# Kernel tuning notes

Hardware: AMD Instinct MI355X
Metric: run time of the kernel (lower is better)

Reference implementation:

```python
import jax, jax.numpy as jnp
import numpy as np

NEG_SLOPE = 0.01

def setup_inputs() -> dict:
    key = jax.random.key(0)
    ks = jax.random.split(key, 6)
    B, N, IN, OUT = 4, 4096, 256, 128
    x = jax.random.normal(ks[0], (B, N, IN), dtype=jnp.float32)
    # fc: Linear(in, out, bias=False); attn_l/attn_r: Linear(out, 1) with bias
    W_fc = jax.random.normal(ks[1], (IN, OUT), dtype=jnp.float32) / np.sqrt(IN)
    w_l = jax.random.normal(ks[2], (OUT,), dtype=jnp.float32) / np.sqrt(OUT)
    b_l = jax.random.normal(ks[3], (), dtype=jnp.float32) * 0.01
    w_r = jax.random.normal(ks[4], (OUT,), dtype=jnp.float32) / np.sqrt(OUT)
    b_r = jax.random.normal(ks[5], (), dtype=jnp.float32) * 0.01
    return {"x": x, "W_fc": W_fc, "w_l": w_l, "b_l": b_l, "w_r": w_r, "b_r": b_r}

def reference(x, W_fc, w_l, b_l, w_r, b_r):
    # feats: [B, N, OUT]
    feats = jnp.einsum('bni,io->bno', x, W_fc)
    f1 = jnp.einsum('bno,o->bn', feats, w_l) + b_l  # [B, N]
    f2 = jnp.einsum('bno,o->bn', feats, w_r) + b_r  # [B, N]
    # logits[b, i, j] = f1[b, i] + f2[b, j]  (broadcast-add)
    logits = f1[:, :, None] + f2[:, None, :]        # [B, N, N]
    scores = jnp.where(logits >= 0, logits, NEG_SLOPE * logits)
    coefs = jax.nn.softmax(scores, axis=1)          # softmax over dim=1, as in torch code
    return jnp.einsum('bij,bjo->bio', coefs, feats) # [B, N, OUT]
```

## Files before the change

### kernel.cpp

```cpp
#include <hip/hip_runtime.h>

using u16 = unsigned short;
using u32 = unsigned int;
using u64 = unsigned long long;

typedef short bf16x8 __attribute__((ext_vector_type(8)));
typedef float f32x4 __attribute__((ext_vector_type(4)));

static constexpr int NB  = 4;
static constexpr int NN  = 4096;
static constexpr int KIN = 256;
static constexpr int FO  = 128;
static constexpr int NROW = NB * NN;
static constexpr int NCC = 64;
static constexpr float SLOPE = 0.01f;

__device__ __forceinline__ u16 f2bf(float f) {
  const u32 u = __float_as_uint(f);
  return (u16)((u + 0x7fffu + ((u >> 16) & 1u)) >> 16);
}
__device__ __forceinline__ float bf2f(u16 h) {
  return __uint_as_float(((u32)h) << 16);
}
__device__ __forceinline__ float dot4(const float4& a, const float4& b) {
  return a.x * b.x + a.y * b.y + a.z * b.z + a.w * b.w;
}

__device__ __forceinline__ u32 f2key(float f) {
  const u32 b = __float_as_uint(f);
  return (b & 0x80000000u) ? ~b : (b | 0x80000000u);
}
__device__ __forceinline__ float key2f(u32 u) {
  const u32 b = (u & 0x80000000u) ? (u ^ 0x80000000u) : ~u;
  return __uint_as_float(b);
}

__device__ __forceinline__ u64 shfl_xor64(u64 v, int m) {
  const u32 lo = __shfl_xor((u32)(v & 0xffffffffu), m, 64);
  const u32 hi = __shfl_xor((u32)(v >> 32), m, 64);
  return ((u64)hi << 32) | (u64)lo;
}
__device__ __forceinline__ void cswap(u64& a, u64& b, bool up) {
  if ((a > b) == up) { const u64 tmp = a; a = b; b = tmp; }
}

__device__ __forceinline__ void reg_session(u64 e[4], int t, int k) {
  const int jstart = (k > 256) ? 128 : (k >> 1);
  for (int j = jstart; j >= 4; j >>= 1) {
    const int J = j >> 2;
    const bool up   = ((t & (k >> 2)) == 0);
    const bool lowr = ((t & J) == 0);
#pragma unroll
    for (int r = 0; r < 4; ++r) {
      const u64 o = shfl_xor64(e[r], J);
      const bool less = e[r] < o;
      e[r] = ((lowr == up) == less) ? e[r] : o;
    }
  }
  if (k >= 4) {
    const bool up = ((t & (k >> 2)) == 0);
    cswap(e[0], e[2], up); cswap(e[1], e[3], up);
  }
  {
    const bool up0 = (((4 * t)     & k) == 0);
    const bool up1 = (((4 * t + 2) & k) == 0);
    cswap(e[0], e[1], up0); cswap(e[2], e[3], up1);
  }
}

__global__ __launch_bounds__(256) void k0_prep(const float* __restrict__ W,
                                               const float* __restrict__ wl,
                                               const float* __restrict__ wr,
                                               float* __restrict__ u_l,
                                               float* __restrict__ u_r,
                                               u16* __restrict__ whT,
                                               u16* __restrict__ wloT) {
  const int t = threadIdx.x;
  const int blk = blockIdx.x;
  if (blk < 64) {
    const int k = blk * 4 + (t >> 6);
    const int lane = t & 63;
    const float w0 = W[k * FO + lane], w1 = W[k * FO + 64 + lane];
    float a1 = w0 * wl[lane] + w1 * wl[64 + lane];
    float a2 = w0 * wr[lane] + w1 * wr[64 + lane];
#pragma unroll
    for (int off = 1; off < 64; off <<= 1) {
      a1 += __shfl_xor(a1, off, 64);
      a2 += __shfl_xor(a2, off, 64);
    }
    if (lane == 0) { u_l[k] = a1; u_r[k] = a2; }
  } else {
#pragma unroll
    for (int e = 0; e < 2; ++e) {
      const int idx = (blk - 64) * 512 + t + e * 256;
      const int col = idx >> 8, k = idx & 255;
      const float v = W[k * FO + col];
      const u16 h = f2bf(v);
      whT[col * KIN + k]  = h;
      wloT[col * KIN + k] = f2bf(v - bf2f(h));
    }
  }
}

__global__ __launch_bounds__(256) void k1_fused(const float* __restrict__ x,
                                                const u16* __restrict__ whT,
                                                const u16* __restrict__ wloT,
                                                const float* __restrict__ u_l,
                                                const float* __restrict__ u_r,
                                                const float* __restrict__ blp,
                                                const float* __restrict__ brp,
                                                float* __restrict__ feats,
                                                float* __restrict__ f1g,
                                                float* __restrict__ f2g) {
  __shared__ u16 axh[64][72];
  __shared__ u16 axl[64][72];
  __shared__ u16 bwh[128][72];
  __shared__ u16 bwl[128][72];
  const int t = threadIdx.x;
  const int w = t >> 6, lane = t & 63;
  const int wm = w >> 1, wn = w & 1;
  const int row0 = blockIdx.x * 64;
  const int xr = t >> 3, xc = t & 7;
  f32x4 acc[2][4];
#pragma unroll
  for (int m = 0; m < 2; ++m)
#pragma unroll
    for (int n = 0; n < 4; ++n) acc[m][n] = (f32x4)0.f;

  float d1a = 0.f, d2a = 0.f, d1b = 0.f, d2b = 0.f;
  float4 xa0, xa1, xb0, xb1;
  bf16x8 wh_[4], wl_[4];

  {
    const float* pa = x + (size_t)(row0 + xr) * KIN + xc * 8;
    const float* pb = x + (size_t)(row0 + xr + 32) * KIN + xc * 8;
    xa0 = *(const float4*)pa; xa1 = *(const float4*)(pa + 4);
    xb0 = *(const float4*)pb; xb1 = *(const float4*)(pb + 4);
#pragma unroll
    for (int i = 0; i < 4; ++i) {
      const int v = t + i * 256;
      const int col = v >> 3, c = v & 7;
      wh_[i] = *(const bf16x8*)(whT + (size_t)col * KIN + c * 8);
      wl_[i] = *(const bf16x8*)(wloT + (size_t)col * KIN + c * 8);
    }
  }

  for (int it = 0; it < 4; ++it) {
    if (it) __syncthreads();
    {
      const float4 ul0 = *(const float4*)(u_l + it * 64 + xc * 8);
      const float4 ul1 = *(const float4*)(u_l + it * 64 + xc * 8 + 4);
      const float4 ur0 = *(const float4*)(u_r + it * 64 + xc * 8);
      const float4 ur1 = *(const float4*)(u_r + it * 64 + xc * 8 + 4);
      d1a += dot4(xa0, ul0) + dot4(xa1, ul1);
      d2a += dot4(xa0, ur0) + dot4(xa1, ur1);
      d1b += dot4(xb0, ul0) + dot4(xb1, ul1);
      d2b += dot4(xb0, ur0) + dot4(xb1, ur1);
    }
    {
      float va[8] = {xa0.x, xa0.y, xa0.z, xa0.w, xa1.x, xa1.y, xa1.z, xa1.w};
      float vb[8] = {xb0.x, xb0.y, xb0.z, xb0.w, xb1.x, xb1.y, xb1.z, xb1.w};
      bf16x8 ha, la, hb, lb;
#pragma unroll
      for (int q = 0; q < 8; ++q) {
        const u16 h1 = f2bf(va[q]);
        ha[q] = (short)h1; la[q] = (short)f2bf(va[q] - bf2f(h1));
        const u16 h2 = f2bf(vb[q]);
        hb[q] = (short)h2; lb[q] = (short)f2bf(vb[q] - bf2f(h2));
      }
      *(bf16x8*)(&axh[xr][xc * 8]) = ha;
      *(bf16x8*)(&axl[xr][xc * 8]) = la;
      *(bf16x8*)(&axh[xr + 32][xc * 8]) = hb;
      *(bf16x8*)(&axl[xr + 32][xc * 8]) = lb;
    }
#pragma unroll
    for (int i = 0; i < 4; ++i) {
      const int v = t + i * 256;
      const int col = v >> 3, c = v & 7;
      *(bf16x8*)(&bwh[col][c * 8]) = wh_[i];
      *(bf16x8*)(&bwl[col][c * 8]) = wl_[i];
    }
    __syncthreads();
    if (it < 3) {
      const float* pa = x + (size_t)(row0 + xr) * KIN + (it + 1) * 64 + xc * 8;
      const float* pb = x + (size_t)(row0 + xr + 32) * KIN + (it + 1) * 64 + xc * 8;
      xa0 = *(const float4*)pa; xa1 = *(const float4*)(pa + 4);
      xb0 = *(const float4*)pb; xb1 = *(const float4*)(pb + 4);
#pragma unroll
      for (int i = 0; i < 4; ++i) {
        const int v = t + i * 256;
        const int col = v >> 3, c = v & 7;
        wh_[i] = *(const bf16x8*)(whT + (size_t)col * KIN + (it + 1) * 64 + c * 8);
        wl_[i] = *(const bf16x8*)(wloT + (size_t)col * KIN + (it + 1) * 64 + c * 8);
      }
    }
#pragma unroll
    for (int kk = 0; kk < 2; ++kk) {
      const int kb = kk * 32 + (lane >> 4) * 8;
      bf16x8 ah[2], al[2], bh[4], blo[4];
#pragma unroll
      for (int m = 0; m < 2; ++m) {
        const int r = wm * 32 + m * 16 + (lane & 15);
        ah[m] = *(const bf16x8*)(&axh[r][kb]);
        al[m] = *(const bf16x8*)(&axl[r][kb]);
      }
#pragma unroll
      for (int n = 0; n < 4; ++n) {
        const int cidx = wn * 64 + n * 16 + (lane & 15);
        bh[n]  = *(const bf16x8*)(&bwh[cidx][kb]);
        blo[n] = *(const bf16x8*)(&bwl[cidx][kb]);
      }
#pragma unroll
      for (int m = 0; m < 2; ++m)
#pragma unroll
        for (int n = 0; n < 4; ++n) {
          acc[m][n] = __builtin_amdgcn_mfma_f32_16x16x32_bf16(ah[m], bh[n],  acc[m][n], 0, 0, 0);
          acc[m][n] = __builtin_amdgcn_mfma_f32_16x16x32_bf16(ah[m], blo[n], acc[m][n], 0, 0, 0);
          acc[m][n] = __builtin_amdgcn_mfma_f32_16x16x32_bf16(al[m], bh[n],  acc[m][n], 0, 0, 0);
        }
    }
  }

#pragma unroll
  for (int m = 0; m < 2; ++m) {
    const int rb = row0 + wm * 32 + m * 16 + (lane >> 4) * 4;
    const int cb = wn * 64 + (lane & 15);
#pragma unroll
    for (int n = 0; n < 4; ++n)
#pragma unroll
      for (int r = 0; r < 4; ++r)
        feats[(size_t)(rb + r) * FO + cb + n * 16] = acc[m][n][r];
  }

#pragma unroll
  for (int off = 1; off < 8; off <<= 1) {
    d1a += __shfl_xor(d1a, off, 64);
    d2a += __shfl_xor(d2a, off, 64);
    d1b += __shfl_xor(d1b, off, 64);
    d2b += __shfl_xor(d2b, off, 64);
  }
  if ((t & 7) == 0) {
    const float bl = blp[0], br = brp[0];
    f1g[row0 + xr] = d1a + bl;
    f2g[row0 + xr] = d2a + br;
    f1g[row0 + xr + 32] = d1b + bl;
    f2g[row0 + xr + 32] = d2b + br;
  }
}

__global__ __launch_bounds__(1024, 1) void k3a_sort(const float* __restrict__ f1g,
                                                    const float* __restrict__ f2g,
                                                    float* __restrict__ f1sort,
                                                    float* __restrict__ sc1,
                                                    float* __restrict__ sc2,
                                                    float* __restrict__ f2sort,
                                                    int* __restrict__ jidxS) {
  __shared__ u64 lds[NN];
  __shared__ float wsumA[16], wsumB[16];
  const int t = threadIdx.x;
  const int lane = t & 63, wv = t >> 6;
  const int b = blockIdx.x & 3;
  const int task = blockIdx.x >> 2;
  const int base = b * NN;
  const float* __restrict__ src = task ? f2g : f1g;

  u64 e[4];
#pragma unroll
  for (int r = 0; r < 4; ++r) {
    const int i = 4 * t + r;
    e[r] = ((u64)f2key(src[base + i]) << 32) | (u32)i;
  }

  for (int k = 2; k <= 256; k <<= 1) reg_session(e, t, k);
#pragma unroll
  for (int r = 0; r < 4; ++r) lds[4 * t + r] = e[r];
  __syncthreads();

  for (int k = 512; k <= NN; k <<= 1) {
    for (int j = k >> 1; j >= 256; j >>= 1) {
#pragma unroll
      for (int pp = 0; pp < 2; ++pp) {
        const int p = t + pp * 1024;
        const int i = ((p & ~(j - 1)) << 1) | (p & (j - 1));
        const int ix = i | j;
        const bool up = ((i & k) == 0);
        const u64 a = lds[i], c = lds[ix];
        if ((a > c) == up) { lds[i] = c; lds[ix] = a; }
      }
      __syncthreads();
    }
#pragma unroll
    for (int r = 0; r < 4; ++r) e[r] = lds[4 * t + r];
    reg_session(e, t, k);
    if (k < NN) {
#pragma unroll
      for (int r = 0; r < 4; ++r) lds[4 * t + r] = e[r];
      __syncthreads();
    }
  }

  if (task == 0) {
    float kf[4], a[4], c[4];
#pragma unroll
    for (int r = 0; r < 4; ++r) {
      kf[r] = key2f((u32)(e[r] >> 32));
      f1sort[base + 4 * t + r] = kf[r];
      a[r] = expf(kf[r]);
      c[r] = expf(SLOPE * kf[r]);
    }
#pragma unroll
    for (int r = 1; r < 4; ++r) { a[r] += a[r - 1]; c[r] += c[r - 1]; }
    const float sa = a[3], sb = c[3];
    float pa = sa, pb = sb;
    for (int off = 1; off < 64; off <<= 1) {
      const float oa = __shfl_up(pa, off, 64);
      const float ob = __shfl_up(pb, off, 64);
      if (lane >= off) { pa += oa; pb += ob; }
    }
    if (lane == 63) { wsumA[wv] = pa; wsumB[wv] = pb; }
    __syncthreads();
    float wpa = 0.f, wpb = 0.f;
    for (int w2 = 0; w2 < wv; ++w2) { wpa += wsumA[w2]; wpb += wsumB[w2]; }
    const float basea = wpa + pa - sa, baseb = wpb + pb - sb;
#pragma unroll
    for (int r = 0; r < 4; ++r) {
      sc1[base + 4 * t + r] = basea + a[r];
      sc2[base + 4 * t + r] = baseb + c[r];
    }
  } else {
#pragma unroll
    for (int r = 0; r < 4; ++r) {
      f2sort[base + 4 * t + r] = key2f((u32)(e[r] >> 32));
      jidxS[base + 4 * t + r]  = (int)(e[r] & 0xffffffffu);
    }
  }
}

__device__ __forceinline__ int lower_bound_s(const float* a, int n, float t) {
  int lo = 0, hi = n;
  while (lo < hi) {
    const int mid = (lo + hi) >> 1;
    if (a[mid] < t) lo = mid + 1; else hi = mid;
  }
  return lo;
}

__global__ __launch_bounds__(512) void k3b_ab(const float* __restrict__ f1sort,
                                              const float* __restrict__ sc1,
                                              const float* __restrict__ sc2,
                                              const float* __restrict__ f2sort,
                                              const float* __restrict__ f1g,
                                              float* __restrict__ alphaS,
                                              float* __restrict__ betaS,
                                              int* __restrict__ kposA,
                                              float* __restrict__ E1g,
                                              float* __restrict__ E2g) {
  __shared__ float s_f1[NN];
  __shared__ float s_f2[NN];
  const int b = blockIdx.x >> 3;
  const int part = blockIdx.x & 7;
  const int base = b * NN;
  for (int i = threadIdx.x; i < NN; i += 512) {
    s_f1[i] = f1sort[base + i];
    s_f2[i] = f2sort[base + i];
  }
  __syncthreads();
  const int g = part * 512 + threadIdx.x;
  const float T1 = sc1[base + NN - 1];
  const float f1max = s_f1[NN - 1];
  {
    const float f2v = s_f2[g];
    const float m = f1max + f2v;
    const float M = (m >= 0.f) ? m : SLOPE * m;
    const int p = lower_bound_s(s_f1, NN, -f2v);
    const float S1 = T1 - (p > 0 ? sc1[base + p - 1] : 0.f);
    const float S2 = (p > 0 ? sc2[base + p - 1] : 0.f);
    const float ea = expf(f2v - M);
    const float eb = expf(SLOPE * f2v - M);
    const float invD = 1.0f / (ea * S1 + eb * S2);
    alphaS[base + g] = ea * invD;
    betaS[base + g]  = eb * invD;
  }
  {
    const float f1v = f1g[base + g];
    kposA[base + g] = lower_bound_s(s_f2, NN, -f1v);
    E1g[base + g] = expf(f1v);
    E2g[base + g] = expf(SLOPE * f1v);
  }
}

__global__ __launch_bounds__(128) void k4a_pref(const float* __restrict__ feats,
                                                const float* __restrict__ alphaS,
                                                const float* __restrict__ betaS,
                                                const int* __restrict__ jidxS,
                                                float* __restrict__ finePreA,
                                                float* __restrict__ finePreB) {
  const int b = blockIdx.x >> 6, cc = blockIdx.x & 63;
  const int o = threadIdx.x;
  const int base = b * NN + cc * 64;
  const float* fb = feats + (size_t)b * NN * FO;
  float accA = 0.f, accB = 0.f;
#pragma unroll 8
  for (int q = 0; q < 64; ++q) {
    const int kk = base + q;
    const int j = jidxS[kk];
    const float fv = fb[(size_t)j * FO + o];
    accA = fmaf(alphaS[kk], fv, accA);
    accB = fmaf(betaS[kk], fv, accB);
    finePreA[(size_t)kk * FO + o] = accA;
    finePreB[(size_t)kk * FO + o] = accB;
  }
}

__global__ __launch_bounds__(128) void k4c_coar(const float* __restrict__ finePreA,
                                                const float* __restrict__ finePreB,
                                                float* __restrict__ coarA,
                                                float* __restrict__ coarB) {
  const int b = blockIdx.x;
  const int o = threadIdx.x;
  float runA = 0.f, runB = 0.f;
#pragma unroll
  for (int c = 0; c < NCC; ++c) {
    coarA[(size_t)(b * (NCC + 1) + c) * FO + o] = runA;
    coarB[(size_t)(b * (NCC + 1) + c) * FO + o] = runB;
    runA += finePreA[(size_t)(b * NN + c * 64 + 63) * FO + o];
    runB += finePreB[(size_t)(b * NN + c * 64 + 63) * FO + o];
  }
  coarA[(size_t)(b * (NCC + 1) + NCC) * FO + o] = runA;
  coarB[(size_t)(b * (NCC + 1) + NCC) * FO + o] = runB;
}

__global__ __launch_bounds__(256) void k5_out(const float* __restrict__ finePreA,
                                              const float* __restrict__ finePreB,
                                              const float* __restrict__ coarA,
                                              const float* __restrict__ coarB,
                                              const int* __restrict__ kposA,
                                              const float* __restrict__ E1g,
                                              const float* __restrict__ E2g,
                                              float* __restrict__ out) {
  const int t = threadIdx.x;
  const int row = blockIdx.x * 2 + (t >> 7);
  const int o = t & 127;
  const int b = row >> 12;
  const int kp = kposA[row];
  const float e1 = E1g[row], e2 = E2g[row];
  const int c = kp >> 6;

  float runA = coarA[(size_t)(b * (NCC + 1) + c) * FO + o];
  float runB = coarB[(size_t)(b * (NCC + 1) + c) * FO + o];
  const float totA = coarA[(size_t)(b * (NCC + 1) + NCC) * FO + o];
  if (kp & 63) {
    runA += finePreA[(size_t)(b * NN + kp - 1) * FO + o];
    runB += finePreB[(size_t)(b * NN + kp - 1) * FO + o];
  }
  out[(size_t)row * FO + o] = fmaf(e1, totA - runA, e2 * runB);
}

extern "C" void kernel_launch(void* const* d_in, const int* in_sizes, int n_in,
                              void* d_out, int out_size, void* d_ws, size_t ws_size,
                              hipStream_t stream) {
  const float* x  = (const float*)d_in[0];
  const float* W  = (const float*)d_in[1];
  const float* wl = (const float*)d_in[2];
  const float* bl = (const float*)d_in[3];
  const float* wr = (const float*)d_in[4];
  const float* br = (const float*)d_in[5];
  float* out = (float*)d_out;

  float* ws = (float*)d_ws;
  float* feats    = ws; ws += NROW * FO;
  float* finePreA = ws; ws += NROW * FO;
  float* finePreB = ws; ws += NROW * FO;
  float* f1g      = ws; ws += NROW;
  float* f2g      = ws; ws += NROW;
  float* f1sort   = ws; ws += NROW;
  float* f2sort   = ws; ws += NROW;
  float* sc1      = ws; ws += NROW;
  float* sc2      = ws; ws += NROW;
  float* alphaS   = ws; ws += NROW;
  float* betaS    = ws; ws += NROW;
  float* E1g      = ws; ws += NROW;
  float* E2g      = ws; ws += NROW;
  int* jidxS      = (int*)ws; ws += NROW;
  int* kposA      = (int*)ws; ws += NROW;
  float* coarA    = ws; ws += NB * (NCC + 1) * FO;
  float* coarB    = ws; ws += NB * (NCC + 1) * FO;
  float* u_l      = ws; ws += KIN;
  float* u_r      = ws; ws += KIN;
  u16* whT  = (u16*)ws; ws += FO * KIN / 2;
  u16* wloT = (u16*)ws; ws += FO * KIN / 2;
  (void)in_sizes; (void)n_in; (void)out_size; (void)ws_size;

  hipLaunchKernelGGL(k0_prep,  dim3(128),       dim3(256),  0, stream,
                     W, wl, wr, u_l, u_r, whT, wloT);
  hipLaunchKernelGGL(k1_fused, dim3(NROW / 64), dim3(256),  0, stream,
                     x, whT, wloT, u_l, u_r, bl, br, feats, f1g, f2g);
  hipLaunchKernelGGL(k3a_sort, dim3(8),         dim3(1024), 0, stream,
                     f1g, f2g, f1sort, sc1, sc2, f2sort, jidxS);
  hipLaunchKernelGGL(k3b_ab,   dim3(NB * 8),    dim3(512),  0, stream,
                     f1sort, sc1, sc2, f2sort, f1g, alphaS, betaS, kposA, E1g, E2g);
  hipLaunchKernelGGL(k4a_pref, dim3(NB * NCC),  dim3(128),  0, stream,
                     feats, alphaS, betaS, jidxS, finePreA, finePreB);
  hipLaunchKernelGGL(k4c_coar, dim3(NB),        dim3(128),  0, stream,
                     finePreA, finePreB, coarA, coarB);
  hipLaunchKernelGGL(k5_out,   dim3(NROW / 2),  dim3(256),  0, stream,
                     finePreA, finePreB, coarA, coarB, kposA, E1g, E2g, out);
}
```

Before: 68.51 us.

## Overlap f1/f2 sort with feature GEMM by merging into one heterogeneous kernel

After: 70.77 us. 1.03x slower.

```diff
diff --git a/kernel.cpp b/kernel.cpp
--- a/kernel.cpp
+++ b/kernel.cpp
@@ -68,31 +68,34 @@
   }
 }
 
-__global__ __launch_bounds__(256) void k0_prep(const float* __restrict__ W,
+__device__ __forceinline__ int lower_bound_s(const float* a, int n, float t) {
+  int lo = 0, hi = n;
+  while (lo < hi) {
+    const int mid = (lo + hi) >> 1;
+    if (a[mid] < t) lo = mid + 1; else hi = mid;
+  }
+  return lo;
+}
+
+__global__ __launch_bounds__(256) void k0_prep(const float* __restrict__ x,
+                                               const float* __restrict__ W,
                                                const float* __restrict__ wl,
+                                               const float* __restrict__ blp,
                                                const float* __restrict__ wr,
-                                               float* __restrict__ u_l,
-                                               float* __restrict__ u_r,
+                                               const float* __restrict__ brp,
                                                u16* __restrict__ whT,
-                                               u16* __restrict__ wloT) {
+                                               u16* __restrict__ wloT,
+                                               float* __restrict__ f1g,
+                                               float* __restrict__ f2g) {
+  __shared__ float uls[KIN];
+  __shared__ float urs[KIN];
   const int t = threadIdx.x;
-  const int blk = blockIdx.x;
-  if (blk < 64) {
-    const int k = blk * 4 + (t >> 6);
-    const int lane = t & 63;
-    const float w0 = W[k * FO + lane], w1 = W[k * FO + 64 + lane];
-    float a1 = w0 * wl[lane] + w1 * wl[64 + lane];
-    float a2 = w0 * wr[lane] + w1 * wr[64 + lane];
-#pragma unroll
-    for (int off = 1; off < 64; off <<= 1) {
-      a1 += __shfl_xor(a1, off, 64);
-      a2 += __shfl_xor(a2, off, 64);
-    }
-    if (lane == 0) { u_l[k] = a1; u_r[k] = a2; }
-  } else {
+  const int bid = blockIdx.x;
+
+  if (bid < 64) {
 #pragma unroll
     for (int e = 0; e < 2; ++e) {
-      const int idx = (blk - 64) * 512 + t + e * 256;
+      const int idx = bid * 512 + t + e * 256;
       const int col = idx >> 8, k = idx & 255;
       const float v = W[k * FO + col];
       const u16 h = f2bf(v);
@@ -100,249 +103,193 @@
       wloT[col * KIN + k] = f2bf(v - bf2f(h));
     }
   }
-}
-
-__global__ __launch_bounds__(256) void k1_fused(const float* __restrict__ x,
-                                                const u16* __restrict__ whT,
-                                                const u16* __restrict__ wloT,
-                                                const float* __restrict__ u_l,
-                                                const float* __restrict__ u_r,
-                                                const float* __restrict__ blp,
-                                                const float* __restrict__ brp,
-                                                float* __restrict__ feats,
-                                                float* __restrict__ f1g,
-                                                float* __restrict__ f2g) {
-  __shared__ u16 axh[64][72];
-  __shared__ u16 axl[64][72];
-  __shared__ u16 bwh[128][72];
-  __shared__ u16 bwl[128][72];
-  const int t = threadIdx.x;
-  const int w = t >> 6, lane = t & 63;
-  const int wm = w >> 1, wn = w & 1;
-  const int row0 = blockIdx.x * 64;
-  const int xr = t >> 3, xc = t & 7;
-  f32x4 acc[2][4];
-#pragma unroll
-  for (int m = 0; m < 2; ++m)
-#pragma unroll
-    for (int n = 0; n < 4; ++n) acc[m][n] = (f32x4)0.f;
-
-  float d1a = 0.f, d2a = 0.f, d1b = 0.f, d2b = 0.f;
-  float4 xa0, xa1, xb0, xb1;
-  bf16x8 wh_[4], wl_[4];
-
   {
-    const float* pa = x + (size_t)(row0 + xr) * KIN + xc * 8;
-    const float* pb = x + (size_t)(row0 + xr + 32) * KIN + xc * 8;
-    xa0 = *(const float4*)pa; xa1 = *(const float4*)(pa + 4);
-    xb0 = *(const float4*)pb; xb1 = *(const float4*)(pb + 4);
-#pragma unroll
-    for (int i = 0; i < 4; ++i) {
-      const int v = t + i * 256;
-      const int col = v >> 3, c = v & 7;
-      wh_[i] = *(const bf16x8*)(whT + (size_t)col * KIN + c * 8);
-      wl_[i] = *(const bf16x8*)(wloT + (size_t)col * KIN + c * 8);
-    }
-  }
-
-  for (int it = 0; it < 4; ++it) {
-    if (it) __syncthreads();
-    {
-      const float4 ul0 = *(const float4*)(u_l + it * 64 + xc * 8);
-      const float4 ul1 = *(const float4*)(u_l + it * 64 + xc * 8 + 4);
-      const float4 ur0 = *(const float4*)(u_r + it * 64 + xc * 8);
-      const float4 ur1 = *(const float4*)(u_r + it * 64 + xc * 8 + 4);
-      d1a += dot4(xa0, ul0) + dot4(xa1, ul1);
-      d2a += dot4(xa0, ur0) + dot4(xa1, ur1);
-      d1b += dot4(xb0, ul0) + dot4(xb1, ul1);
-      d2b += dot4(xb0, ur0) + dot4(xb1, ur1);
-    }
-    {
-      float va[8] = {xa0.x, xa0.y, xa0.z, xa0.w, xa1.x, xa1.y, xa1.z, xa1.w};
-      float vb[8] = {xb0.x, xb0.y, xb0.z, xb0.w, xb1.x, xb1.y, xb1.z, xb1.w};
-      bf16x8 ha, la, hb, lb;
-#pragma unroll
-      for (int q = 0; q < 8; ++q) {
-        const u16 h1 = f2bf(va[q]);
-        ha[q] = (short)h1; la[q] = (short)f2bf(va[q] - bf2f(h1));
-        const u16 h2 = f2bf(vb[q]);
-        hb[q] = (short)h2; lb[q] = (short)f2bf(vb[q] - bf2f(h2));
-      }
-      *(bf16x8*)(&axh[xr][xc * 8]) = ha;
-      *(bf16x8*)(&axl[xr][xc * 8]) = la;
-      *(bf16x8*)(&axh[xr + 32][xc * 8]) = hb;
-      *(bf16x8*)(&axl[xr + 32][xc * 8]) = lb;
-    }
-#pragma unroll
-    for (int i = 0; i < 4; ++i) {
-      const int v = t + i * 256;
-      const int col = v >> 3, c = v & 7;
-      *(bf16x8*)(&bwh[col][c * 8]) = wh_[i];
-      *(bf16x8*)(&bwl[col][c * 8]) = wl_[i];
-    }
+    const float* Wr = W + (size_t)t * FO;
+    float s1 = 0.f, s2 = 0.f;
+#pragma unroll 8
+    for (int c = 0; c < FO; ++c) {
+      const float wv = Wr[c];
+      s1 = fmaf(wv, wl[c], s1);
+      s2 = fmaf(wv, wr[c], s2);
+    }
+    uls[t] = s1; urs[t] = s2;
+  }
+  __syncthreads();
+  const int wv = t >> 6, lane = t & 63;
+  const int row0 = bid * 64 + wv * 16;
+  const float4 ul = *(const float4*)(&uls[lane * 4]);
+  const float4 ur = *(const float4*)(&urs[lane * 4]);
+  const float blv = blp[0], brv = brp[0];
+  for (int r = 0; r < 16; ++r) {
+    const int row = row0 + r;
+    const float4 xv = *(const float4*)(x + (size_t)row * KIN + lane * 4);
+    float d1 = dot4(xv, ul);
+    float d2 = dot4(xv, ur);
+#pragma unroll
+    for (int off = 1; off < 64; off <<= 1) {
+      d1 += __shfl_xor(d1, off, 64);
+      d2 += __shfl_xor(d2, off, 64);
+    }
+    if (lane == 0) { f1g[row] = d1 + blv; f2g[row] = d2 + brv; }
+  }
+}
+
+__global__ __launch_bounds__(1024, 1) void kB_main(const float* __restrict__ x,
+                                                   const u16* __restrict__ whT,
+                                                   const u16* __restrict__ wloT,
+                                                   const float* __restrict__ f1g,
+                                                   const float* __restrict__ f2g,
+                                                   float* __restrict__ feats,
+                                                   float* __restrict__ f1sort,
+                                                   float* __restrict__ sc1,
+                                                   float* __restrict__ sc2,
+                                                   float* __restrict__ f2sort,
+                                                   int* __restrict__ jidxS) {
+  __shared__ __align__(16) unsigned char smem[55296];
+  const int tid = threadIdx.x;
+  const int bid = blockIdx.x;
+
+  if (bid < 8) {
+    u64* lds = (u64*)smem;
+    float* wsumA = (float*)(smem + 32768);
+    float* wsumB = (float*)(smem + 32832);
+    const int t = tid;
+    const int lane = t & 63, wv = t >> 6;
+    const int b = bid & 3;
+    const int task = bid >> 2;
+    const int base = b * NN;
+    const float* __restrict__ src = task ? f2g : f1g;
+
+    u64 e[4];
+#pragma unroll
+    for (int r = 0; r < 4; ++r) {
+      const int i = 4 * t + r;
+      e[r] = ((u64)f2key(src[base + i]) << 32) | (u32)i;
+    }
+    for (int k = 2; k <= 256; k <<= 1) reg_session(e, t, k);
+#pragma unroll
+    for (int r = 0; r < 4; ++r) lds[4 * t + r] = e[r];
     __syncthreads();
-    if (it < 3) {
-      const float* pa = x + (size_t)(row0 + xr) * KIN + (it + 1) * 64 + xc * 8;
-      const float* pb = x + (size_t)(row0 + xr + 32) * KIN + (it + 1) * 64 + xc * 8;
-      xa0 = *(const float4*)pa; xa1 = *(const float4*)(pa + 4);
-      xb0 = *(const float4*)pb; xb1 = *(const float4*)(pb + 4);
-#pragma unroll
-      for (int i = 0; i < 4; ++i) {
-        const int v = t + i * 256;
-        const int col = v >> 3, c = v & 7;
-        wh_[i] = *(const bf16x8*)(whT + (size_t)col * KIN + (it + 1) * 64 + c * 8);
-        wl_[i] = *(const bf16x8*)(wloT + (size_t)col * KIN + (it + 1) * 64 + c * 8);
-      }
-    }
-#pragma unroll
-    for (int kk = 0; kk < 2; ++kk) {
-      const int kb = kk * 32 + (lane >> 4) * 8;
-      bf16x8 ah[2], al[2], bh[4], blo[4];
-#pragma unroll
-      for (int m = 0; m < 2; ++m) {
-        const int r = wm * 32 + m * 16 + (lane & 15);
-        ah[m] = *(const bf16x8*)(&axh[r][kb]);
-        al[m] = *(const bf16x8*)(&axl[r][kb]);
-      }
-#pragma unroll
-      for (int n = 0; n < 4; ++n) {
-        const int cidx = wn * 64 + n * 16 + (lane & 15);
-        bh[n]  = *(const bf16x8*)(&bwh[cidx][kb]);
-        blo[n] = *(const bf16x8*)(&bwl[cidx][kb]);
-      }
-#pragma unroll
-      for (int m = 0; m < 2; ++m)
-#pragma unroll
-        for (int n = 0; n < 4; ++n) {
-          acc[m][n] = __builtin_amdgcn_mfma_f32_16x16x32_bf16(ah[m], bh[n],  acc[m][n], 0, 0, 0);
-          acc[m][n] = __builtin_amdgcn_mfma_f32_16x16x32_bf16(ah[m], blo[n], acc[m][n], 0, 0, 0);
-          acc[m][n] = __builtin_amdgcn_mfma_f32_16x16x32_bf16(al[m], bh[n],  acc[m][n], 0, 0, 0);
+    for (int k = 512; k <= NN; k <<= 1) {
+      for (int j = k >> 1; j >= 256; j >>= 1) {
+#pragma unroll
+        for (int pp = 0; pp < 2; ++pp) {
+          const int pw = t + pp * 1024;
+          const int i = ((pw & ~(j - 1)) << 1) | (pw & (j - 1));
+          const int ix = i | j;
+          const bool up = ((i & k) == 0);
+          const u64 a = lds[i], c = lds[ix];
+          if ((a > c) == up) { lds[i] = c; lds[ix] = a; }
         }
-    }
-  }
-
-#pragma unroll
-  for (int m = 0; m < 2; ++m) {
-    const int rb = row0 + wm * 32 + m * 16 + (lane >> 4) * 4;
-    const int cb = wn * 64 + (lane & 15);
-#pragma unroll
-    for (int n = 0; n < 4; ++n)
+        __syncthreads();
+      }
+#pragma unroll
+      for (int r = 0; r < 4; ++r) e[r] = lds[4 * t + r];
+      reg_session(e, t, k);
+      if (k < NN) {
+#pragma unroll
+        for (int r = 0; r < 4; ++r) lds[4 * t + r] = e[r];
+        __syncthreads();
+      }
+    }
+    if (task == 0) {
+      float kf[4], a[4], c[4];
+#pragma unroll
+      for (int r = 0; r < 4; ++r) {
+        kf[r] = key2f((u32)(e[r] >> 32));
+        f1sort[base + 4 * t + r] = kf[r];
+        a[r] = expf(kf[r]);
+        c[r] = expf(SLOPE * kf[r]);
+      }
+#pragma unroll
+      for (int r = 1; r < 4; ++r) { a[r] += a[r - 1]; c[r] += c[r - 1]; }
+      const float sa = a[3], sb = c[3];
+      float pa = sa, pb = sb;
+      for (int off = 1; off < 64; off <<= 1) {
+        const float oa = __shfl_up(pa, off, 64);
+        const float ob = __shfl_up(pb, off, 64);
+        if (lane >= off) { pa += oa; pb += ob; }
+      }
+      if (lane == 63) { wsumA[wv] = pa; wsumB[wv] = pb; }
+      __syncthreads();
+      float wpa = 0.f, wpb = 0.f;
+      for (int w2 = 0; w2 < wv; ++w2) { wpa += wsumA[w2]; wpb += wsumB[w2]; }
+      const float basea = wpa + pa - sa, baseb = wpb + pb - sb;
+#pragma unroll
+      for (int r = 0; r < 4; ++r) {
+        sc1[base + 4 * t + r] = basea + a[r];
+        sc2[base + 4 * t + r] = baseb + c[r];
+      }
+    } else {
+#pragma unroll
+      for (int r = 0; r < 4; ++r) {
+        f2sort[base + 4 * t + r] = key2f((u32)(e[r] >> 32));
+        jidxS[base + 4 * t + r]  = (int)(e[r] & 0xffffffffu);
+      }
+    }
+  } else {
+    u16* axh = (u16*)smem;
+    u16* axl = (u16*)(smem + 9216);
+    u16* bwh = (u16*)(smem + 18432);
+    u16* bwl = (u16*)(smem + 36864);
+    const int w = tid >> 6, lane = tid & 63;
+    const int wm = w >> 2, wn = w & 3;
+    const int row0 = (bid - 8) * 64;
+    const int xr = tid >> 4, xc4 = (tid & 15) * 4;
+    const int wcol = tid >> 3, wc = tid & 7;
+    f32x4 acc[2];
+    acc[0] = (f32x4)0.f; acc[1] = (f32x4)0.f;
+    float4 xv;
+    bf16x8 whb, wlb;
+    xv  = *(const float4*)(x + (size_t)(row0 + xr) * KIN + xc4);
+    whb = *(const bf16x8*)(whT  + (size_t)wcol * KIN + wc * 8);
+    wlb = *(const bf16x8*)(wloT + (size_t)wcol * KIN + wc * 8);
+
+    for (int it = 0; it < 4; ++it) {
+      if (it) __syncthreads();
+      {
+        float va[4] = {xv.x, xv.y, xv.z, xv.w};
+        ushort4 hh, ll;
+        const u16 h0 = f2bf(va[0]); hh.x = h0; ll.x = f2bf(va[0] - bf2f(h0));
+        const u16 h1 = f2bf(va[1]); hh.y = h1; ll.y = f2bf(va[1] - bf2f(h1));
+        const u16 h2 = f2bf(va[2]); hh.z = h2; ll.z = f2bf(va[2] - bf2f(h2));
+        const u16 h3 = f2bf(va[3]); hh.w = h3; ll.w = f2bf(va[3] - bf2f(h3));
+        *(ushort4*)(&axh[xr * 72 + xc4]) = hh;
+        *(ushort4*)(&axl[xr * 72 + xc4]) = ll;
+      }
+      *(bf16x8*)(&bwh[wcol * 72 + wc * 8]) = whb;
+      *(bf16x8*)(&bwl[wcol * 72 + wc * 8]) = wlb;
+      __syncthreads();
+      if (it < 3) {
+        xv  = *(const float4*)(x + (size_t)(row0 + xr) * KIN + (it + 1) * 64 + xc4);
+        whb = *(const bf16x8*)(whT  + (size_t)wcol * KIN + (it + 1) * 64 + wc * 8);
+        wlb = *(const bf16x8*)(wloT + (size_t)wcol * KIN + (it + 1) * 64 + wc * 8);
+      }
+#pragma unroll
+      for (int kk = 0; kk < 2; ++kk) {
+        const int kb = kk * 32 + (lane >> 4) * 8;
+        const int ar = wm * 16 + (lane & 15);
+        const bf16x8 ah = *(const bf16x8*)(&axh[ar * 72 + kb]);
+        const bf16x8 al = *(const bf16x8*)(&axl[ar * 72 + kb]);
+#pragma unroll
+        for (int n = 0; n < 2; ++n) {
+          const int cidx = wn * 32 + n * 16 + (lane & 15);
+          const bf16x8 bh  = *(const bf16x8*)(&bwh[cidx * 72 + kb]);
+          const bf16x8 blo = *(const bf16x8*)(&bwl[cidx * 72 + kb]);
+          acc[n] = __builtin_amdgcn_mfma_f32_16x16x32_bf16(ah, bh,  acc[n], 0, 0, 0);
+          acc[n] = __builtin_amdgcn_mfma_f32_16x16x32_bf16(ah, blo, acc[n], 0, 0, 0);
+          acc[n] = __builtin_amdgcn_mfma_f32_16x16x32_bf16(al, bh,  acc[n], 0, 0, 0);
+        }
+      }
+    }
+    const int rb = row0 + wm * 16 + (lane >> 4) * 4;
+    const int cb = wn * 32 + (lane & 15);
+#pragma unroll
+    for (int n = 0; n < 2; ++n)
 #pragma unroll
       for (int r = 0; r < 4; ++r)
-        feats[(size_t)(rb + r) * FO + cb + n * 16] = acc[m][n][r];
-  }
-
-#pragma unroll
-  for (int off = 1; off < 8; off <<= 1) {
-    d1a += __shfl_xor(d1a, off, 64);
-    d2a += __shfl_xor(d2a, off, 64);
-    d1b += __shfl_xor(d1b, off, 64);
-    d2b += __shfl_xor(d2b, off, 64);
-  }
-  if ((t & 7) == 0) {
-    const float bl = blp[0], br = brp[0];
-    f1g[row0 + xr] = d1a + bl;
-    f2g[row0 + xr] = d2a + br;
-    f1g[row0 + xr + 32] = d1b + bl;
-    f2g[row0 + xr + 32] = d2b + br;
-  }
-}
-
-__global__ __launch_bounds__(1024, 1) void k3a_sort(const float* __restrict__ f1g,
-                                                    const float* __restrict__ f2g,
-                                                    float* __restrict__ f1sort,
-                                                    float* __restrict__ sc1,
-                                                    float* __restrict__ sc2,
-                                                    float* __restrict__ f2sort,
-                                                    int* __restrict__ jidxS) {
-  __shared__ u64 lds[NN];
-  __shared__ float wsumA[16], wsumB[16];
-  const int t = threadIdx.x;
-  const int lane = t & 63, wv = t >> 6;
-  const int b = blockIdx.x & 3;
-  const int task = blockIdx.x >> 2;
-  const int base = b * NN;
-  const float* __restrict__ src = task ? f2g : f1g;
-
-  u64 e[4];
-#pragma unroll
-  for (int r = 0; r < 4; ++r) {
-    const int i = 4 * t + r;
-    e[r] = ((u64)f2key(src[base + i]) << 32) | (u32)i;
-  }
-
-  for (int k = 2; k <= 256; k <<= 1) reg_session(e, t, k);
-#pragma unroll
-  for (int r = 0; r < 4; ++r) lds[4 * t + r] = e[r];
-  __syncthreads();
-
-  for (int k = 512; k <= NN; k <<= 1) {
-    for (int j = k >> 1; j >= 256; j >>= 1) {
-#pragma unroll
-      for (int pp = 0; pp < 2; ++pp) {
-        const int p = t + pp * 1024;
-        const int i = ((p & ~(j - 1)) << 1) | (p & (j - 1));
-        const int ix = i | j;
-        const bool up = ((i & k) == 0);
-        const u64 a = lds[i], c = lds[ix];
-        if ((a > c) == up) { lds[i] = c; lds[ix] = a; }
-      }
-      __syncthreads();
-    }
-#pragma unroll
-    for (int r = 0; r < 4; ++r) e[r] = lds[4 * t + r];
-    reg_session(e, t, k);
-    if (k < NN) {
-#pragma unroll
-      for (int r = 0; r < 4; ++r) lds[4 * t + r] = e[r];
-      __syncthreads();
-    }
-  }
-
-  if (task == 0) {
-    float kf[4], a[4], c[4];
-#pragma unroll
-    for (int r = 0; r < 4; ++r) {
-      kf[r] = key2f((u32)(e[r] >> 32));
-      f1sort[base + 4 * t + r] = kf[r];
-      a[r] = expf(kf[r]);
-      c[r] = expf(SLOPE * kf[r]);
-    }
-#pragma unroll
-    for (int r = 1; r < 4; ++r) { a[r] += a[r - 1]; c[r] += c[r - 1]; }
-    const float sa = a[3], sb = c[3];
-    float pa = sa, pb = sb;
-    for (int off = 1; off < 64; off <<= 1) {
-      const float oa = __shfl_up(pa, off, 64);
-      const float ob = __shfl_up(pb, off, 64);
-      if (lane >= off) { pa += oa; pb += ob; }
-    }
-    if (lane == 63) { wsumA[wv] = pa; wsumB[wv] = pb; }
-    __syncthreads();
-    float wpa = 0.f, wpb = 0.f;
-    for (int w2 = 0; w2 < wv; ++w2) { wpa += wsumA[w2]; wpb += wsumB[w2]; }
-    const float basea = wpa + pa - sa, baseb = wpb + pb - sb;
-#pragma unroll
-    for (int r = 0; r < 4; ++r) {
-      sc1[base + 4 * t + r] = basea + a[r];
-      sc2[base + 4 * t + r] = baseb + c[r];
-    }
-  } else {
-#pragma unroll
-    for (int r = 0; r < 4; ++r) {
-      f2sort[base + 4 * t + r] = key2f((u32)(e[r] >> 32));
-      jidxS[base + 4 * t + r]  = (int)(e[r] & 0xffffffffu);
-    }
-  }
-}
-
-__device__ __forceinline__ int lower_bound_s(const float* a, int n, float t) {
-  int lo = 0, hi = n;
-  while (lo < hi) {
-    const int mid = (lo + hi) >> 1;
-    if (a[mid] < t) lo = mid + 1; else hi = mid;
-  }
-  return lo;
+        feats[(size_t)(rb + r) * FO + cb + n * 16] = acc[n][r];
+  }
 }
 
 __global__ __launch_bounds__(512) void k3b_ab(const float* __restrict__ f1sort,
@@ -485,24 +432,21 @@
   int* kposA      = (int*)ws; ws += NROW;
   float* coarA    = ws; ws += NB * (NCC + 1) * FO;
   float* coarB    = ws; ws += NB * (NCC + 1) * FO;
-  float* u_l      = ws; ws += KIN;
-  float* u_r      = ws; ws += KIN;
   u16* whT  = (u16*)ws; ws += FO * KIN / 2;
   u16* wloT = (u16*)ws; ws += FO * KIN / 2;
   (void)in_sizes; (void)n_in; (void)out_size; (void)ws_size;
 
-  hipLaunchKernelGGL(k0_prep,  dim3(128),       dim3(256),  0, stream,
-                     W, wl, wr, u_l, u_r, whT, wloT);
-  hipLaunchKernelGGL(k1_fused, dim3(NROW / 64), dim3(256),  0, stream,
-                     x, whT, wloT, u_l, u_r, bl, br, feats, f1g, f2g);
-  hipLaunchKernelGGL(k3a_sort, dim3(8),         dim3(1024), 0, stream,
-                     f1g, f2g, f1sort, sc1, sc2, f2sort, jidxS);
-  hipLaunchKernelGGL(k3b_ab,   dim3(NB * 8),    dim3(512),  0, stream,
+  hipLaunchKernelGGL(k0_prep,  dim3(NROW / 64),     dim3(256),  0, stream,
+                     x, W, wl, bl, wr, br, whT, wloT, f1g, f2g);
+  hipLaunchKernelGGL(kB_main,  dim3(8 + NROW / 64), dim3(1024), 0, stream,
+                     x, whT, wloT, f1g, f2g, feats,
+                     f1sort, sc1, sc2, f2sort, jidxS);
+  hipLaunchKernelGGL(k3b_ab,   dim3(NB * 8),        dim3(512),  0, stream,
                      f1sort, sc1, sc2, f2sort, f1g, alphaS, betaS, kposA, E1g, E2g);
-  hipLaunchKernelGGL(k4a_pref, dim3(NB * NCC),  dim3(128),  0, stream,
+  hipLaunchKernelGGL(k4a_pref, dim3(NB * NCC),      dim3(128),  0, stream,
                      feats, alphaS, betaS, jidxS, finePreA, finePreB);
-  hipLaunchKernelGGL(k4c_coar, dim3(NB),        dim3(128),  0, stream,
+  hipLaunchKernelGGL(k4c_coar, dim3(NB),            dim3(128),  0, stream,
                      finePreA, finePreB, coarA, coarB);
-  hipLaunchKernelGGL(k5_out,   dim3(NROW / 2),  dim3(256),  0, stream,
+  hipLaunchKernelGGL(k5_out,   dim3(NROW / 2),      dim3(256),  0, stream,
                      finePreA, finePreB, coarA, coarB, kposA, E1g, E2g, out);
 }
```
